# Kernel optimization log

Hardware: AMD Instinct MI355X
Metric: run time of the kernel (lower is better)

Reference implementation:

```python
import jax, jax.numpy as jnp
import numpy as np

N_THRESHOLDS = 10


def setup_inputs() -> dict:
    key = jax.random.key(0)
    k1, k2, k3 = jax.random.split(key, 3)
    shape = (32, 1024, 1024)
    prediction = jax.random.normal(k1, shape, dtype=jnp.float32)
    mask = jax.random.randint(k2, shape, 0, 2, dtype=jnp.int32)
    target = jax.random.randint(k3, shape, 0, 2, dtype=jnp.int32)
    return {"prediction": prediction, "mask": mask, "target": target}


def reference(prediction, mask, target):
    # thresholds = linspace(0,1,n+2)[1:-1], same as the torch module
    thresholds = jnp.linspace(0.0, 1.0, N_THRESHOLDS + 2, dtype=jnp.float32)[1:-1]

    s = jax.nn.sigmoid(prediction).ravel()            # [N]
    m = mask.ravel().astype(bool)                     # [N] valid mask
    t = target.ravel().astype(bool)                   # [N]
    mt = m & t                                        # masked positives

    # Broadcast compare against all thresholds at once (single fused pass,
    # no per-threshold host sync like the original loop).
    pos = s[None, :] > thresholds[:, None]            # [T, N] bool

    tp = jnp.sum(pos & mt[None, :], axis=1)           # [T] int32
    p = jnp.sum(pos & m[None, :], axis=1)             # predicted-positive count

    total_m = jnp.sum(m)                              # total valid elements
    total_t = jnp.sum(mt)                             # total true positives in mask

    fp = p - tp
    fn = total_t - tp
    tn = total_m - p - fn

    # classes layout matches torch module: rows = [tp, fp, tn, fn]
    return jnp.stack([tp, fp, tn, fn], axis=0).astype(jnp.float32)
```

## Files before the change

### kernel.cpp

```cpp
#include <hip/hip_runtime.h>


#define NTHR 10
#define NBKT 11
#define NCNT 22
#define WS_STRIDE 16

__device__ __forceinline__ unsigned wave_reduce_add(unsigned v) {
#pragma unroll
    for (int off = 32; off > 0; off >>= 1)
        v += __shfl_down(v, off, 64);
    return v;
}

__global__ __launch_bounds__(64) void zero_ws_kernel(unsigned* __restrict__ ws) {
    int i = threadIdx.x;
    if (i < NCNT) ws[i * WS_STRIDE] = 0u;
}

__device__ __forceinline__ void proc_elem(float pv, unsigned mm, unsigned tt,
                                          const float* L,
                                          unsigned long long& hP,
                                          unsigned long long& hT) {
    unsigned mt = mm & tt;
    unsigned b = 0u;
#pragma unroll
    for (int j = 0; j < NTHR; ++j) b += (pv > L[j]) ? 1u : 0u;
    unsigned sh = (b << 2) + b;
    hP += (unsigned long long)mm << sh;
    hT += (unsigned long long)mt << sh;
}

__device__ __forceinline__ void flush_hist(unsigned long long& hP,
                                           unsigned long long& hT,
                                           unsigned* cP, unsigned* cT) {
#pragma unroll
    for (int b = 0; b < NBKT; ++b) {
        cP[b] += (unsigned)(hP >> (5 * b)) & 31u;
        cT[b] += (unsigned)(hT >> (5 * b)) & 31u;
    }
    hP = 0ull; hT = 0ull;
}

__global__ __launch_bounds__(256) void count_kernel(
        const float4* __restrict__ pred4,
        const int4*  __restrict__ mask4,
        const int4*  __restrict__ targ4,
        const float* __restrict__ pred,
        const int*   __restrict__ mask,
        const int*   __restrict__ targ,
        unsigned* __restrict__ ws, int half, int n) {
    const float L[NTHR] = {-2.3025851f, -1.5040774f, -0.98082925f, -0.55961579f,
                           -0.18232156f, 0.18232156f,  0.55961579f,  0.98082925f,
                            1.5040774f,  2.3025851f};
    unsigned cP[NBKT] = {}, cT[NBKT] = {};
    unsigned long long hP = 0ull, hT = 0ull;

    const int idx    = blockIdx.x * blockDim.x + threadIdx.x;
    const int stride = gridDim.x * blockDim.x;

    int fcnt = 0;
    for (int i = idx; i < half; i += stride) {
        float4 p0 = pred4[i];
        float4 p1 = pred4[i + half];
        int4   m0 = mask4[i];
        int4   m1 = mask4[i + half];
        int4   t0 = targ4[i];
        int4   t1 = targ4[i + half];

        proc_elem(p0.x, (unsigned)m0.x, (unsigned)t0.x, L, hP, hT);
        proc_elem(p0.y, (unsigned)m0.y, (unsigned)t0.y, L, hP, hT);
        proc_elem(p0.z, (unsigned)m0.z, (unsigned)t0.z, L, hP, hT);
        proc_elem(p0.w, (unsigned)m0.w, (unsigned)t0.w, L, hP, hT);
        proc_elem(p1.x, (unsigned)m1.x, (unsigned)t1.x, L, hP, hT);
        proc_elem(p1.y, (unsigned)m1.y, (unsigned)t1.y, L, hP, hT);
        proc_elem(p1.z, (unsigned)m1.z, (unsigned)t1.z, L, hP, hT);
        proc_elem(p1.w, (unsigned)m1.w, (unsigned)t1.w, L, hP, hT);

        if (++fcnt == 3) { flush_hist(hP, hT, cP, cT); fcnt = 0; }
    }
    flush_hist(hP, hT, cP, cT);

    {
        int tail_base = half * 8;
        int i = tail_base + idx;
        if (i < n) {
            proc_elem(pred[i], (unsigned)mask[i], (unsigned)targ[i], L, hP, hT);
            flush_hist(hP, hT, cP, cT);
        }
    }

    unsigned vals[NCNT];
#pragma unroll
    for (int b = 0; b < NBKT; ++b) { vals[b] = cP[b]; vals[NBKT + b] = cT[b]; }
#pragma unroll
    for (int c = 0; c < NCNT; ++c) vals[c] = wave_reduce_add(vals[c]);

    __shared__ unsigned partial[4][NCNT];
    const int wave = threadIdx.x >> 6;
    const int lane = threadIdx.x & 63;
    if (lane == 0) {
#pragma unroll
        for (int c = 0; c < NCNT; ++c) partial[wave][c] = vals[c];
    }
    __syncthreads();
    if (threadIdx.x < NCNT) {
        unsigned s = partial[0][threadIdx.x] + partial[1][threadIdx.x] +
                     partial[2][threadIdx.x] + partial[3][threadIdx.x];
        atomicAdd(&ws[threadIdx.x * WS_STRIDE], s);
    }
}

__global__ __launch_bounds__(64) void finalize_kernel(const unsigned* __restrict__ ws,
                                                      float* __restrict__ out) {
    int j = threadIdx.x;
    if (j < NTHR) {
        unsigned totM = 0u, totT = 0u, p = 0u, tp = 0u;
#pragma unroll
        for (int b = 0; b < NBKT; ++b) {
            unsigned vP = ws[b * WS_STRIDE];
            unsigned vT = ws[(NBKT + b) * WS_STRIDE];
            totM += vP; totT += vT;
            if (b > j) { p += vP; tp += vT; }
        }
        unsigned fp = p - tp;
        unsigned fn = totT - tp;
        unsigned tn = totM - p - fn;
        out[j]            = (float)tp;
        out[NTHR + j]     = (float)fp;
        out[2 * NTHR + j] = (float)tn;
        out[3 * NTHR + j] = (float)fn;
    }
}

extern "C" void kernel_launch(void* const* d_in, const int* in_sizes, int n_in,
                              void* d_out, int out_size, void* d_ws, size_t ws_size,
                              hipStream_t stream) {
    const float* pred = (const float*)d_in[0];
    const int*   mask = (const int*)d_in[1];
    const int*   targ = (const int*)d_in[2];
    unsigned*    ws   = (unsigned*)d_ws;
    float*       out  = (float*)d_out;

    const int n    = in_sizes[0];
    const int nvec = n / 4;
    const int half = nvec / 2;

    zero_ws_kernel<<<1, 64, 0, stream>>>(ws);

    const int blocks = 2048;
    count_kernel<<<blocks, 256, 0, stream>>>(
        (const float4*)pred, (const int4*)mask, (const int4*)targ,
        pred, mask, targ, ws, half, n);

    finalize_kernel<<<1, 64, 0, stream>>>(ws, out);
}
```

Measured before the change: 362.9 us.

## Use wave-contiguous 4-chunk loads and packed 10-bit per-thread bucket counters

Each wave now handles a contiguous 256-float4 tile per iteration. Every lane issues four float4/int4 loads per array before computing, so more loads are in flight than in the old two-halves split. The 22 per-thread bucket counters are packed into four 64-bit words with 10-bit fields, which cuts register use. The packed fields only stay correct while each thread processes at most 1023 elements, so the scheme depends on the problem size and grid size.

```diff
diff --git a/kernel.cpp b/kernel.cpp
--- a/kernel.cpp
+++ b/kernel.cpp
@@ -18,10 +18,12 @@
     if (i < NCNT) ws[i * WS_STRIDE] = 0u;
 }
 
-__device__ __forceinline__ void proc_elem(float pv, unsigned mm, unsigned tt,
-                                          const float* L,
-                                          unsigned long long& hP,
-                                          unsigned long long& hT) {
+__device__ __forceinline__ void acc_elem(float pv, unsigned mm, unsigned tt,
+                                         unsigned long long& hP,
+                                         unsigned long long& hT) {
+    const float L[NTHR] = {-2.3025851f, -1.5040774f, -0.98082925f, -0.55961579f,
+                           -0.18232156f, 0.18232156f,  0.55961579f,  0.98082925f,
+                            1.5040774f,  2.3025851f};
     unsigned mt = mm & tt;
     unsigned b = 0u;
 #pragma unroll
@@ -31,13 +33,27 @@
     hT += (unsigned long long)mt << sh;
 }
 
-__device__ __forceinline__ void flush_hist(unsigned long long& hP,
-                                           unsigned long long& hT,
-                                           unsigned* cP, unsigned* cT) {
+__device__ __forceinline__ void acc_vec(const float4& p, const int4& m, const int4& t,
+                                        unsigned long long& hP,
+                                        unsigned long long& hT) {
+    acc_elem(p.x, (unsigned)m.x, (unsigned)t.x, hP, hT);
+    acc_elem(p.y, (unsigned)m.y, (unsigned)t.y, hP, hT);
+    acc_elem(p.z, (unsigned)m.z, (unsigned)t.z, hP, hT);
+    acc_elem(p.w, (unsigned)m.w, (unsigned)t.w, hP, hT);
+}
+
+__device__ __forceinline__ void flush_hist(unsigned long long& hP, unsigned long long& hT,
+                                           unsigned long long& Plo, unsigned long long& Phi,
+                                           unsigned long long& Tlo, unsigned long long& Thi) {
 #pragma unroll
-    for (int b = 0; b < NBKT; ++b) {
-        cP[b] += (unsigned)(hP >> (5 * b)) & 31u;
-        cT[b] += (unsigned)(hT >> (5 * b)) & 31u;
+    for (int b = 0; b < 6; ++b) {
+        Plo += (unsigned long long)((unsigned)(hP >> (5 * b)) & 31u) << (10 * b);
+        Tlo += (unsigned long long)((unsigned)(hT >> (5 * b)) & 31u) << (10 * b);
+    }
+#pragma unroll
+    for (int b = 6; b < NBKT; ++b) {
+        Phi += (unsigned long long)((unsigned)(hP >> (5 * b)) & 31u) << (10 * (b - 6));
+        Thi += (unsigned long long)((unsigned)(hT >> (5 * b)) & 31u) << (10 * (b - 6));
     }
     hP = 0ull; hT = 0ull;
 }
@@ -49,57 +65,71 @@
         const float* __restrict__ pred,
         const int*   __restrict__ mask,
         const int*   __restrict__ targ,
-        unsigned* __restrict__ ws, int half, int n) {
-    const float L[NTHR] = {-2.3025851f, -1.5040774f, -0.98082925f, -0.55961579f,
-                           -0.18232156f, 0.18232156f,  0.55961579f,  0.98082925f,
-                            1.5040774f,  2.3025851f};
-    unsigned cP[NBKT] = {}, cT[NBKT] = {};
-    unsigned long long hP = 0ull, hT = 0ull;
+        unsigned* __restrict__ ws, int nvec, int n) {
+    unsigned long long Plo = 0ull, Phi = 0ull, Tlo = 0ull, Thi = 0ull;
 
-    const int idx    = blockIdx.x * blockDim.x + threadIdx.x;
-    const int stride = gridDim.x * blockDim.x;
+    const int tid    = blockIdx.x * blockDim.x + threadIdx.x;
+    const int lane   = tid & 63;
+    const int waveId = tid >> 6;
+    const int totalWaves = (gridDim.x * blockDim.x) >> 6;
+    const int strideG    = totalWaves << 8;
 
-    int fcnt = 0;
-    for (int i = idx; i < half; i += stride) {
-        float4 p0 = pred4[i];
-        float4 p1 = pred4[i + half];
-        int4   m0 = mask4[i];
-        int4   m1 = mask4[i + half];
-        int4   t0 = targ4[i];
-        int4   t1 = targ4[i + half];
-
-        proc_elem(p0.x, (unsigned)m0.x, (unsigned)t0.x, L, hP, hT);
-        proc_elem(p0.y, (unsigned)m0.y, (unsigned)t0.y, L, hP, hT);
-        proc_elem(p0.z, (unsigned)m0.z, (unsigned)t0.z, L, hP, hT);
-        proc_elem(p0.w, (unsigned)m0.w, (unsigned)t0.w, L, hP, hT);
-        proc_elem(p1.x, (unsigned)m1.x, (unsigned)t1.x, L, hP, hT);
-        proc_elem(p1.y, (unsigned)m1.y, (unsigned)t1.y, L, hP, hT);
-        proc_elem(p1.z, (unsigned)m1.z, (unsigned)t1.z, L, hP, hT);
-        proc_elem(p1.w, (unsigned)m1.w, (unsigned)t1.w, L, hP, hT);
-
-        if (++fcnt == 3) { flush_hist(hP, hT, cP, cT); fcnt = 0; }
+    for (int base = waveId << 8; base < nvec; base += strideG) {
+        unsigned long long hP = 0ull, hT = 0ull;
+        if (base + 256 <= nvec) {
+            float4 p0 = pred4[base +        lane];
+            float4 p1 = pred4[base +  64  + lane];
+            float4 p2 = pred4[base + 128  + lane];
+            float4 p3 = pred4[base + 192  + lane];
+            int4   m0 = mask4[base +        lane];
+            int4   m1 = mask4[base +  64  + lane];
+            int4   m2 = mask4[base + 128  + lane];
+            int4   m3 = mask4[base + 192  + lane];
+            int4   t0 = targ4[base +        lane];
+            int4   t1 = targ4[base +  64  + lane];
+            int4   t2 = targ4[base + 128  + lane];
+            int4   t3 = targ4[base + 192  + lane];
+            acc_vec(p0, m0, t0, hP, hT);
+            acc_vec(p1, m1, t1, hP, hT);
+            acc_vec(p2, m2, t2, hP, hT);
+            acc_vec(p3, m3, t3, hP, hT);
+        } else {
+#pragma unroll
+            for (int c = 0; c < 4; ++c) {
+                int g = base + (c << 6) + lane;
+                if (g < nvec)
+                    acc_vec(pred4[g], mask4[g], targ4[g], hP, hT);
+            }
+        }
+        flush_hist(hP, hT, Plo, Phi, Tlo, Thi);
     }
-    flush_hist(hP, hT, cP, cT);
 
     {
-        int tail_base = half * 8;
-        int i = tail_base + idx;
+        int i = nvec * 4 + tid;
         if (i < n) {
-            proc_elem(pred[i], (unsigned)mask[i], (unsigned)targ[i], L, hP, hT);
-            flush_hist(hP, hT, cP, cT);
+            unsigned long long hP = 0ull, hT = 0ull;
+            acc_elem(pred[i], (unsigned)mask[i], (unsigned)targ[i], hP, hT);
+            flush_hist(hP, hT, Plo, Phi, Tlo, Thi);
         }
     }
 
     unsigned vals[NCNT];
 #pragma unroll
-    for (int b = 0; b < NBKT; ++b) { vals[b] = cP[b]; vals[NBKT + b] = cT[b]; }
+    for (int b = 0; b < 6; ++b) {
+        vals[b]        = (unsigned)(Plo >> (10 * b)) & 1023u;
+        vals[NBKT + b] = (unsigned)(Tlo >> (10 * b)) & 1023u;
+    }
+#pragma unroll
+    for (int b = 6; b < NBKT; ++b) {
+        vals[b]        = (unsigned)(Phi >> (10 * (b - 6))) & 1023u;
+        vals[NBKT + b] = (unsigned)(Thi >> (10 * (b - 6))) & 1023u;
+    }
 #pragma unroll
     for (int c = 0; c < NCNT; ++c) vals[c] = wave_reduce_add(vals[c]);
 
     __shared__ unsigned partial[4][NCNT];
     const int wave = threadIdx.x >> 6;
-    const int lane = threadIdx.x & 63;
-    if (lane == 0) {
+    if ((threadIdx.x & 63) == 0) {
 #pragma unroll
         for (int c = 0; c < NCNT; ++c) partial[wave][c] = vals[c];
     }
@@ -144,14 +174,13 @@
 
     const int n    = in_sizes[0];
     const int nvec = n / 4;
-    const int half = nvec / 2;
 
     zero_ws_kernel<<<1, 64, 0, stream>>>(ws);
 
     const int blocks = 2048;
     count_kernel<<<blocks, 256, 0, stream>>>(
         (const float4*)pred, (const int4*)mask, (const int4*)targ,
-        pred, mask, targ, ws, half, n);
+        pred, mask, targ, ws, nvec, n);
 
     finalize_kernel<<<1, 64, 0, stream>>>(ws, out);
 }
```

Result: no change. 356.9 us (-1.6%).
